# Optimization experiments

Measured on AMD Instinct MI355X. Metric: run time of the kernel, lower is better.

## Reference

```python
import jax, jax.numpy as jnp
import numpy as np

B, T, D = 8, 4096, 1024
H, DH = 16, 64  # n_heads, d_head = D // H
EPS = 1e-12


def setup_inputs() -> dict:
    key = jax.random.key(0)
    k0, k1, k2, k3 = jax.random.split(key, 4)
    x = jax.random.normal(k0, (B, T, D), jnp.float32)
    # reach: xavier_uniform gain=0.01 -> tiny weights; approximate with scaled normal
    Wr = jax.random.normal(k1, (D, D), jnp.float32) * (0.01 / np.sqrt(D))
    br = jnp.zeros((D,), jnp.float32)
    # forget: xavier_uniform gain=1
    Wf = jax.random.normal(k2, (D, D), jnp.float32) * (1.0 / np.sqrt(D))
    bf = jnp.zeros((D,), jnp.float32)
    scale = jnp.ones((1, H, DH), jnp.float32)
    res_gate = jax.random.normal(k3, (1, H, DH), jnp.float32) * 0.01
    return {"x": x, "Wr": Wr, "br": br, "Wf": Wf, "bf": bf,
            "scale": scale, "res_gate": res_gate}


def reference(x, Wr, br, Wf, bf, scale, res_gate):
    Bv, Tv, Dv = x.shape
    # projections (nn.Linear applies x @ W.T + b)
    v = jnp.tanh(x @ Wr.T + br).reshape(Bv, Tv, H, DH)          # [B,T,H,DH]
    alpha = jax.nn.sigmoid(x @ Wf.T + bf).reshape(Bv, Tv, H, DH)
    # time-major for scan
    vt = jnp.moveaxis(v, 1, 0)      # [T,B,H,DH]
    at = jnp.moveaxis(alpha, 1, 0)  # [T,B,H,DH]

    def step(state, inp):
        a_t, v_t = inp
        s = state * a_t + (1.0 - a_t) * v_t
        rms = jnp.sqrt(jnp.mean(s * s, axis=-1, keepdims=True) + EPS)
        final = s / rms * scale + v_t * res_gate
        # note: state for next step is the gated/normed output (as in source)
        return final, final

    init = jnp.zeros((Bv, H, DH), x.dtype)
    _, out = jax.lax.scan(step, init, (at, vt))   # out: [T,B,H,DH]
    return jnp.moveaxis(out, 0, 1).reshape(Bv, Tv, Dv)
```

## Files before the change

kernel.cpp:

```cpp
#include <hip/hip_runtime.h>
#include <hip/hip_bf16.h>
#include <math.h>

#define B_DIM 8
#define T_DIM 4096
#define D_DIM 1024
#define H_DIM 16
#define DH_DIM 64
#define M_TOT (B_DIM * T_DIM)
#define K_DIM 1024
#define N_DIM 1024
#define EPS_F 1e-12f

typedef __attribute__((ext_vector_type(8))) short short8;
typedef __attribute__((ext_vector_type(4))) float f32x4;

__global__ __launch_bounds__(256) void split_bf16_kernel(const float* __restrict__ in,
                                                         __hip_bfloat16* __restrict__ hi,
                                                         __hip_bfloat16* __restrict__ lo,
                                                         int n4) {
    int i = blockIdx.x * blockDim.x + threadIdx.x;
    int stride = gridDim.x * blockDim.x;
    for (; i < n4; i += stride) {
        float4 f = ((const float4*)in)[i];
        union { ushort4 u; __hip_bfloat16 h[4]; } ch, cl;
        #pragma unroll
        for (int j = 0; j < 4; ++j) {
            float fj = ((const float*)&f)[j];
            __hip_bfloat16 hv = __float2bfloat16(fj);
            ch.h[j] = hv;
            cl.h[j] = __float2bfloat16(fj - __bfloat162float(hv));
        }
        ((ushort4*)hi)[i] = ch.u;
        ((ushort4*)lo)[i] = cl.u;
    }
}

#define BM 128
#define BN 128
#define BK 64

__device__ __forceinline__ void gload_lds16(const void* g, void* l) {
    __builtin_amdgcn_global_load_lds(
        (const __attribute__((address_space(1))) unsigned int*)g,
        (__attribute__((address_space(3))) unsigned int*)l,
        16, 0, 0);
}

__global__ __launch_bounds__(256) void gemm_proj_kernel(
    const __hip_bfloat16* __restrict__ Xh, const __hip_bfloat16* __restrict__ Xl,
    const __hip_bfloat16* __restrict__ WrH, const __hip_bfloat16* __restrict__ WrL,
    const __hip_bfloat16* __restrict__ WfH, const __hip_bfloat16* __restrict__ WfL,
    const float* __restrict__ br, const float* __restrict__ bfv,
    float* __restrict__ Vout,
    float* __restrict__ Aout)
{
    __shared__ __align__(16) __hip_bfloat16 Ah[BM * BK];
    __shared__ __align__(16) __hip_bfloat16 Al[BM * BK];
    __shared__ __align__(16) __hip_bfloat16 Bh[BN * BK];
    __shared__ __align__(16) __hip_bfloat16 Bl[BN * BK];

    const int bid = blockIdx.x;
    const int bm = bid >> 4;
    const int py = bid & 15;
    const int which = py >> 3;
    const int bn = py & 7;
    const __hip_bfloat16* Wh = which ? WfH : WrH;
    const __hip_bfloat16* Wl = which ? WfL : WrL;
    const float* bias = which ? bfv : br;

    const int tid = threadIdx.x;
    const int lane = tid & 63;
    const int w = tid >> 6;
    const int wm = w >> 1, wn = w & 1;

    f32x4 acc[4][4] = {};

    const size_t arow0 = (size_t)bm * BM;
    const size_t brow0 = (size_t)bn * BN;

    for (int kt = 0; kt < K_DIM; kt += BK) {
        __syncthreads();
        #pragma unroll
        for (int i = 0; i < 4; ++i) {
            const int c = (w * 4 + i) * 64 + lane;
            const int row = c >> 3;
            const int ch  = c & 7;
            const size_t ga = (arow0 + row) * K_DIM + kt + ch * 8;
            const size_t gb = (brow0 + row) * K_DIM + kt + ch * 8;
            gload_lds16(Xh + ga, &Ah[c * 8]);
            gload_lds16(Xl + ga, &Al[c * 8]);
            gload_lds16(Wh + gb, &Bh[c * 8]);
            gload_lds16(Wl + gb, &Bl[c * 8]);
        }
        __syncthreads();

        #pragma unroll
        for (int kk = 0; kk < BK; kk += 32) {
            short8 ah[4], al[4], bh[4], bl[4];
            const int koff = kk + ((lane >> 4) * 8);
            #pragma unroll
            for (int f = 0; f < 4; ++f) {
                const int ar = wm * 64 + f * 16 + (lane & 15);
                ah[f] = *(const short8*)&Ah[ar * BK + koff];
                al[f] = *(const short8*)&Al[ar * BK + koff];
                const int brr = wn * 64 + f * 16 + (lane & 15);
                bh[f] = *(const short8*)&Bh[brr * BK + koff];
                bl[f] = *(const short8*)&Bl[brr * BK + koff];
            }
            #pragma unroll
            for (int fm = 0; fm < 4; ++fm)
                #pragma unroll
                for (int fn = 0; fn < 4; ++fn) {
                    acc[fm][fn] = __builtin_amdgcn_mfma_f32_16x16x32_bf16(
                        ah[fm], bh[fn], acc[fm][fn], 0, 0, 0);
                    acc[fm][fn] = __builtin_amdgcn_mfma_f32_16x16x32_bf16(
                        ah[fm], bl[fn], acc[fm][fn], 0, 0, 0);
                    acc[fm][fn] = __builtin_amdgcn_mfma_f32_16x16x32_bf16(
                        al[fm], bh[fn], acc[fm][fn], 0, 0, 0);
                }
        }
    }

    const int col = lane & 15;
    const int rowb = (lane >> 4) * 4;
    #pragma unroll
    for (int fm = 0; fm < 4; ++fm) {
        #pragma unroll
        for (int fn = 0; fn < 4; ++fn) {
            const size_t gn = brow0 + wn * 64 + fn * 16 + col;
            const float bia = bias[gn];
            #pragma unroll
            for (int r = 0; r < 4; ++r) {
                const size_t gm = arow0 + wm * 64 + fm * 16 + rowb + r;
                const float val = acc[fm][fn][r] + bia;
                if (which == 0) {
                    Vout[gm * N_DIM + gn] = tanhf(val);
                } else {
                    Aout[gm * N_DIM + gn] = 1.0f / (1.0f + __expf(-val));
                }
            }
        }
    }
}

template<int CTRL>
__device__ __forceinline__ float dpp_add(float x) {
    return x + __int_as_float(__builtin_amdgcn_update_dpp(
        0, __float_as_int(x), CTRL, 0xf, 0xf, false));
}

__device__ __forceinline__ float bfly_sum64(float x) {
    x = dpp_add<0xB1>(x);
    x = dpp_add<0x4E>(x);
    x = dpp_add<0x141>(x);
    x = dpp_add<0x140>(x);
#if __has_builtin(__builtin_amdgcn_permlane16_swap) && __has_builtin(__builtin_amdgcn_permlane32_swap)
    {
        unsigned int xu = __float_as_uint(x);
        auto r16 = __builtin_amdgcn_permlane16_swap(xu, xu, false, false);
        x = __uint_as_float(r16[0]) + __uint_as_float(r16[1]);
        unsigned int yu = __float_as_uint(x);
        auto r32 = __builtin_amdgcn_permlane32_swap(yu, yu, false, false);
        x = __uint_as_float(r32[0]) + __uint_as_float(r32[1]);
        return x;
    }
#else
    {
        int v = __float_as_int(x);
        x += __int_as_float(__builtin_amdgcn_update_dpp(0, v, 0x142, 0xa, 0xf, false));
        v = __float_as_int(x);
        x += __int_as_float(__builtin_amdgcn_update_dpp(0, v, 0x143, 0xc, 0xf, false));
        return __int_as_float(__builtin_amdgcn_readlane(__float_as_int(x), 63));
    }
#endif
}

#define PF 16

__global__ __launch_bounds__(64) void scan_kernel(
    float* __restrict__ vout,
    const float* __restrict__ abuf,
    const float* __restrict__ scale,
    const float* __restrict__ res_gate)
{
    const int bh = blockIdx.x;
    const int b = bh >> 4, h = bh & 15;
    const int lane = threadIdx.x;
    const size_t base = ((size_t)b * T_DIM) * D_DIM + h * DH_DIM + lane;
    const float sc = scale[h * DH_DIM + lane];
    const float rg = res_gate[h * DH_DIM + lane];
    const float sc8 = 8.0f * sc;

    float sig = 0.0f;
    float inv = 0.0f;
    float wprev = 0.0f;

    float vc[PF], ac[PF];
    #pragma unroll
    for (int i = 0; i < PF; ++i) {
        vc[i] = vout[base + (size_t)i * D_DIM];
        ac[i] = abuf[base + (size_t)i * D_DIM];
    }

    for (int t0 = 0; t0 < T_DIM; t0 += PF) {
        float vn[PF], an[PF];
        const int t1 = t0 + PF;
        if (t1 < T_DIM) {
            #pragma unroll
            for (int i = 0; i < PF; ++i) {
                vn[i] = vout[base + (size_t)(t1 + i) * D_DIM];
                an[i] = abuf[base + (size_t)(t1 + i) * D_DIM];
            }
        } else {
            #pragma unroll
            for (int i = 0; i < PF; ++i) { vn[i] = 0.0f; an[i] = 0.0f; }
        }
        #pragma unroll
        for (int i = 0; i < PF; ++i) {
            const float a  = ac[i], vv = vc[i];
            const float g  = a * sc;
            const float cc = fmaf(a, wprev - vv, vv) * 0.125f;
            wprev = vv * rg;
            const float p  = g * sig;
            sig = fmaf(inv, p, cc);
            const float T  = bfly_sum64(sig * sig);
            inv = __builtin_amdgcn_rsqf(T + EPS_F);
            const float f  = fmaf(inv, sig * sc8, wprev);
            vout[base + (size_t)(t0 + i) * D_DIM] = f;
        }
        #pragma unroll
        for (int i = 0; i < PF; ++i) { vc[i] = vn[i]; ac[i] = an[i]; }
    }
}

extern "C" void kernel_launch(void* const* d_in, const int* in_sizes, int n_in,
                              void* d_out, int out_size, void* d_ws, size_t ws_size,
                              hipStream_t stream) {
    const float* x     = (const float*)d_in[0];
    const float* Wr    = (const float*)d_in[1];
    const float* br    = (const float*)d_in[2];
    const float* Wf    = (const float*)d_in[3];
    const float* bf    = (const float*)d_in[4];
    const float* scale = (const float*)d_in[5];
    const float* rgate = (const float*)d_in[6];
    float* out = (float*)d_out;

    char* ws = (char*)d_ws;
    __hip_bfloat16* x_hi  = (__hip_bfloat16*)(ws);
    __hip_bfloat16* x_lo  = (__hip_bfloat16*)(ws + 67108864);
    __hip_bfloat16* wr_hi = (__hip_bfloat16*)(ws + 134217728);
    __hip_bfloat16* wr_lo = (__hip_bfloat16*)(ws + 136314880);
    __hip_bfloat16* wf_hi = (__hip_bfloat16*)(ws + 138412032);
    __hip_bfloat16* wf_lo = (__hip_bfloat16*)(ws + 140509184);
    float*          a_f32 = (float*)(ws + 142606336);

    split_bf16_kernel<<<2048, 256, 0, stream>>>(x,  x_hi,  x_lo,  (M_TOT * K_DIM) / 4);
    split_bf16_kernel<<<512,  256, 0, stream>>>(Wr, wr_hi, wr_lo, (N_DIM * K_DIM) / 4);
    split_bf16_kernel<<<512,  256, 0, stream>>>(Wf, wf_hi, wf_lo, (N_DIM * K_DIM) / 4);

    gemm_proj_kernel<<<4096, 256, 0, stream>>>(
        x_hi, x_lo, wr_hi, wr_lo, wf_hi, wf_lo, br, bf, out, a_f32);

    scan_kernel<<<B_DIM * H_DIM, 64, 0, stream>>>(out, a_f32, scale, rgate);
}
```

Before: 1.178 ms.

## Double-buffer scan prefetch with inline-asm loads and explicit vmcnt waits

Rewrites the scan kernel's prefetch as a ping-pong double buffer. Loads are issued through inline-asm global_load_dword, and each step waits with an explicit s_waitcnt vmcnt plus a sched_barrier. The aim is to stop the compiler from inserting conservative waits that serialise the next chunk's loads with the current chunk's recurrence. The hand-set vmcnt(16) must match the number of outstanding loads and stores. Because the asm is volatile with memory clobbers, the compiler's scheduling freedom is reduced.

```diff
diff --git a/kernel.cpp b/kernel.cpp
--- a/kernel.cpp
+++ b/kernel.cpp
@@ -178,6 +178,21 @@
 
 #define PF 16
 
+#define GLOAD(dst, ptr) asm volatile("global_load_dword %0, %1, off" \
+    : "=v"(dst) : "v"(ptr) : "memory")
+
+#define SCAN_STEP(a_, v_, tidx) do { \
+    const float a  = (a_), vv = (v_); \
+    const float g  = a * sc; \
+    const float cc = fmaf(a, wprev - vv, vv) * 0.125f; \
+    wprev = vv * rg; \
+    const float p  = g * sig; \
+    sig = fmaf(inv, p, cc); \
+    const float Tt = bfly_sum64(sig * sig); \
+    inv = __builtin_amdgcn_rsqf(Tt + EPS_F); \
+    vout[base + (size_t)(tidx) * D_DIM] = fmaf(inv, sig * sc8, wprev); \
+} while (0)
+
 __global__ __launch_bounds__(64) void scan_kernel(
     float* __restrict__ vout,
     const float* __restrict__ abuf,
@@ -192,45 +207,44 @@
     const float rg = res_gate[h * DH_DIM + lane];
     const float sc8 = 8.0f * sc;
 
-    float sig = 0.0f;
-    float inv = 0.0f;
-    float wprev = 0.0f;
-
-    float vc[PF], ac[PF];
+    float sig = 0.0f, inv = 0.0f, wprev = 0.0f;
+
+    float vA[PF], aA[PF], vB[PF], aB[PF];
+
     #pragma unroll
     for (int i = 0; i < PF; ++i) {
-        vc[i] = vout[base + (size_t)i * D_DIM];
-        ac[i] = abuf[base + (size_t)i * D_DIM];
-    }
-
-    for (int t0 = 0; t0 < T_DIM; t0 += PF) {
-        float vn[PF], an[PF];
-        const int t1 = t0 + PF;
-        if (t1 < T_DIM) {
+        GLOAD(vA[i], vout + base + (size_t)i * D_DIM);
+        GLOAD(aA[i], abuf + base + (size_t)i * D_DIM);
+    }
+    asm volatile("s_waitcnt vmcnt(0)" ::: "memory");
+    __builtin_amdgcn_sched_barrier(0);
+
+    for (int t0 = 0; t0 < T_DIM; t0 += 2 * PF) {
+        {
+            const int tn = t0 + PF;
             #pragma unroll
             for (int i = 0; i < PF; ++i) {
-                vn[i] = vout[base + (size_t)(t1 + i) * D_DIM];
-                an[i] = abuf[base + (size_t)(t1 + i) * D_DIM];
-            }
-        } else {
-            #pragma unroll
-            for (int i = 0; i < PF; ++i) { vn[i] = 0.0f; an[i] = 0.0f; }
-        }
-        #pragma unroll
-        for (int i = 0; i < PF; ++i) {
-            const float a  = ac[i], vv = vc[i];
-            const float g  = a * sc;
-            const float cc = fmaf(a, wprev - vv, vv) * 0.125f;
-            wprev = vv * rg;
-            const float p  = g * sig;
-            sig = fmaf(inv, p, cc);
-            const float T  = bfly_sum64(sig * sig);
-            inv = __builtin_amdgcn_rsqf(T + EPS_F);
-            const float f  = fmaf(inv, sig * sc8, wprev);
-            vout[base + (size_t)(t0 + i) * D_DIM] = f;
-        }
-        #pragma unroll
-        for (int i = 0; i < PF; ++i) { vc[i] = vn[i]; ac[i] = an[i]; }
+                GLOAD(vB[i], vout + base + (size_t)(tn + i) * D_DIM);
+                GLOAD(aB[i], abuf + base + (size_t)(tn + i) * D_DIM);
+            }
+            #pragma unroll
+            for (int i = 0; i < PF; ++i) SCAN_STEP(aA[i], vA[i], t0 + i);
+            asm volatile("s_waitcnt vmcnt(16)" ::: "memory");
+            __builtin_amdgcn_sched_barrier(0);
+        }
+        {
+            const int tn = t0 + 2 * PF;
+            #pragma unroll
+            for (int i = 0; i < PF; ++i) {
+                const int t = (tn + i < T_DIM) ? (tn + i) : (T_DIM - 1);
+                GLOAD(vA[i], vout + base + (size_t)t * D_DIM);
+                GLOAD(aA[i], abuf + base + (size_t)t * D_DIM);
+            }
+            #pragma unroll
+            for (int i = 0; i < PF; ++i) SCAN_STEP(aB[i], vB[i], t0 + PF + i);
+            asm volatile("s_waitcnt vmcnt(16)" ::: "memory");
+            __builtin_amdgcn_sched_barrier(0);
+        }
     }
 }
 
```

Result: faster. 1.006 ms (-14.6%).
